# Performance work log

Measured on AMD Instinct MI355X. Metric: run time of the kernel, lower is better.

Reference implementation:

```python
import jax, jax.numpy as jnp
import numpy as np

D_MODEL = 512
PROJ = 2 * D_MODEL  # 1024
N_STATES = 32
KSIZE = 4
LN_EPS = 1e-3  # keras LayerNormalization default epsilon


def setup_inputs() -> dict:
    key = jax.random.key(0)
    ks = jax.random.split(key, 16)
    B, L = 2, 2048
    s_in = 1.0 / np.sqrt(D_MODEL)
    s_pr = 1.0 / np.sqrt(PROJ)
    x = jax.random.normal(ks[0], (B, L, D_MODEL), dtype=jnp.float32)
    # LayerNorm params
    ln_gamma = jnp.ones((D_MODEL,), jnp.float32)
    ln_beta = jnp.zeros((D_MODEL,), jnp.float32)
    # dense1 / dense2: d_model -> proj
    W1 = jax.random.normal(ks[1], (D_MODEL, PROJ), jnp.float32) * s_in
    b1 = jnp.zeros((PROJ,), jnp.float32)
    W2 = jax.random.normal(ks[2], (D_MODEL, PROJ), jnp.float32) * s_in
    b2 = jnp.zeros((PROJ,), jnp.float32)
    # depthwise causal conv1d: kernel (K, 1, PROJ) in WIO layout, groups=PROJ
    conv_k = jax.random.normal(ks[3], (KSIZE, 1, PROJ), jnp.float32) * 0.5
    conv_b = jnp.zeros((PROJ,), jnp.float32)
    # SSM params
    A_log = jnp.log(jnp.broadcast_to(jnp.arange(1, N_STATES + 1, dtype=jnp.float32), (PROJ, N_STATES)))
    D_skip = jnp.ones((PROJ,), jnp.float32)
    WB = jax.random.normal(ks[4], (PROJ, N_STATES), jnp.float32) * s_pr
    bB = jnp.zeros((N_STATES,), jnp.float32)
    WC = jax.random.normal(ks[5], (PROJ, N_STATES), jnp.float32) * s_pr
    bC = jnp.zeros((N_STATES,), jnp.float32)
    Wd = jax.random.normal(ks[6], (PROJ, PROJ), jnp.float32) * s_pr
    bd = jnp.zeros((PROJ,), jnp.float32)
    # dense3: proj -> d_model
    W3 = jax.random.normal(ks[7], (PROJ, D_MODEL), jnp.float32) * s_pr
    b3 = jnp.zeros((D_MODEL,), jnp.float32)
    return dict(x=x, ln_gamma=ln_gamma, ln_beta=ln_beta, W1=W1, b1=b1, W2=W2, b2=b2,
                conv_k=conv_k, conv_b=conv_b, A_log=A_log, D_skip=D_skip,
                WB=WB, bB=bB, WC=WC, bC=bC, Wd=Wd, bd=bd, W3=W3, b3=b3)


def _layernorm(x, gamma, beta):
    mu = jnp.mean(x, axis=-1, keepdims=True)
    var = jnp.mean(jnp.square(x - mu), axis=-1, keepdims=True)
    return (x - mu) * jax.lax.rsqrt(var + LN_EPS) * gamma + beta


def _causal_dwconv(x, k, b):
    # x: [B,L,C], k: [K,1,C], depthwise causal conv (left-pad K-1)
    y = jax.lax.conv_general_dilated(
        x, k, window_strides=(1,), padding=[(KSIZE - 1, 0)],
        dimension_numbers=('NWC', 'WIO', 'NWC'), feature_group_count=PROJ)
    return y + b


def _selective_scan(u, delta, A, Bm, Cm, D_skip):
    # u, delta: [B,L,D]; A: [D,N]; Bm, Cm: [B,L,N]; D_skip: [D]
    deltaA = jnp.einsum('bld,dn->bldn', delta, A)                 # [B,L,D,N]
    deltaBu = jnp.einsum('bld,bld,bln->bldn', delta, u, Bm)        # [B,L,D,N]
    # shift deltaA left by one along L, zero at the end (pad trick in source)
    shifted = jnp.concatenate([deltaA[:, 1:], jnp.zeros_like(deltaA[:, :1])], axis=1)
    # reversed cumsum along L, then exp
    e = jnp.exp(jnp.flip(jnp.cumsum(jnp.flip(shifted, axis=1), axis=1), axis=1))
    xs = jnp.cumsum(deltaBu * e, axis=1) / (e + 1e-12)
    y = jnp.einsum('bldn,bln->bld', xs, Cm)
    return y + u * D_skip


def reference(x, ln_gamma, ln_beta, W1, b1, W2, b2, conv_k, conv_b,
              A_log, D_skip, WB, bB, WC, bC, Wd, bd, W3, b3):
    h = _layernorm(x, ln_gamma, ln_beta)
    x1 = h @ W1 + b1                      # [B,L,PROJ]
    x1 = _causal_dwconv(x1, conv_k, conv_b)
    x1 = jax.nn.silu(x1)
    A = -jnp.exp(A_log)                    # [PROJ,N]
    Cm = x1 @ WC + bC                      # [B,L,N]
    Bm = x1 @ WB + bB                      # [B,L,N]
    delta = jax.nn.softplus(x1 @ Wd + bd)  # [B,L,PROJ]
    y = _selective_scan(x1, delta, A, Bm, Cm, D_skip)
    x2 = jax.nn.silu(h @ W2 + b2)
    out = (y * x2) @ W3 + b3 + x           # residual; dropout is identity at inference
    return out
```

## Files before the change

kernel.cpp:

```cpp
#include <hip/hip_runtime.h>
#include <stdint.h>

#define L_SEQ 2048
#define BATCH 2
#define DMODEL 512
#define PROJ 1024
#define NST 32
#define NCATU 1088
#define ROWS (BATCH*L_SEQ)
#define THRESH 50.0f

typedef float f32x4 __attribute__((ext_vector_type(4)));
typedef short short8 __attribute__((ext_vector_type(8)));

__device__ inline float bf2f(unsigned short u){ uint32_t x=((uint32_t)u)<<16; float f; __builtin_memcpy(&f,&x,4); return f; }
__device__ inline unsigned short f2bf(float f){ uint32_t x; __builtin_memcpy(&x,&f,4); uint32_t r=x+0x7FFFu+((x>>16)&1u); return (unsigned short)(r>>16); }
__device__ inline float siluf(float x){ return x/(1.f+__expf(-x)); }
__device__ inline float softplusf(float x){ return x>20.f? x : log1pf(__expf(x)); }

#define AS1(p) ((const __attribute__((address_space(1))) void*)(p))
#define AS3(p) ((__attribute__((address_space(3))) void*)(p))

template<int N> __device__ inline void wait_vmcnt(){
  if constexpr (N==0)      asm volatile("s_waitcnt vmcnt(0)" ::: "memory");
  else if constexpr (N==4) asm volatile("s_waitcnt vmcnt(4)" ::: "memory");
  else if constexpr (N==8) asm volatile("s_waitcnt vmcnt(8)" ::: "memory");
  else                     asm volatile("s_waitcnt vmcnt(12)" ::: "memory");
}

__global__ __launch_bounds__(256)
void prep_ln_kernel(const float* __restrict__ W1, const float* __restrict__ b1,
                    const float* __restrict__ W2, const float* __restrict__ b2,
                    const float* __restrict__ Wd, const float* __restrict__ bd,
                    const float* __restrict__ WB, const float* __restrict__ bB,
                    const float* __restrict__ WC, const float* __restrict__ bC,
                    const float* __restrict__ W3,
                    unsigned short* __restrict__ W12t, unsigned short* __restrict__ Wcatt,
                    unsigned short* __restrict__ W3t, float* __restrict__ bias12,
                    float* __restrict__ biascat,
                    const float* __restrict__ x, const float* __restrict__ ln_g,
                    const float* __restrict__ ln_b, unsigned short* __restrict__ H)
{
  __shared__ float tile[32][33];
  int bid = blockIdx.x;
  int lx = threadIdx.x & 31, ly = threadIdx.x >> 5;
  if (bid < 1024) {
    int kt = bid & 15, nt = bid >> 4;
    int k0 = kt*32, n0 = nt*32;
    const float* S = (n0 < 1024) ? W1 : W2;
    int nc = (n0 < 1024) ? n0 : n0 - 1024;
#pragma unroll
    for (int i=0;i<4;i++)
      tile[ly+i*8][lx] = S[(size_t)(k0+ly+i*8)*1024 + nc + lx];
    __syncthreads();
#pragma unroll
    for (int i=0;i<4;i++)
      W12t[(size_t)(n0+ly+i*8)*512 + k0 + lx] = f2bf(tile[lx][ly+i*8]);
    return;
  }
  if (bid < 2112) {
    int t = bid - 1024;
    int kt = t & 31, nt = t >> 5;
    int k0 = kt*32, n0 = nt*32;
#pragma unroll
    for (int i=0;i<4;i++){
      int k = k0 + ly + i*8;
      float v;
      if (n0 < 1024)       v = Wd[(size_t)k*1024 + n0 + lx];
      else if (n0 == 1024) v = WB[(size_t)k*32 + lx];
      else                 v = WC[(size_t)k*32 + lx];
      tile[ly+i*8][lx] = v;
    }
    __syncthreads();
#pragma unroll
    for (int i=0;i<4;i++)
      Wcatt[(size_t)(n0+ly+i*8)*1024 + k0 + lx] = f2bf(tile[lx][ly+i*8]);
    return;
  }
  if (bid < 2624) {
    int t = bid - 2112;
    int kt = t & 31, nt = t >> 5;
    int k0 = kt*32, n0 = nt*32;
#pragma unroll
    for (int i=0;i<4;i++)
      tile[ly+i*8][lx] = W3[(size_t)(k0+ly+i*8)*512 + n0 + lx];
    __syncthreads();
#pragma unroll
    for (int i=0;i<4;i++)
      W3t[(size_t)(n0+ly+i*8)*1024 + k0 + lx] = f2bf(tile[lx][ly+i*8]);
    return;
  }
  if (bid < 2637) {
    int j = (bid - 2624)*256 + threadIdx.x;
    if (j < 2048) { bias12[j] = (j < 1024) ? b1[j] : b2[j-1024]; return; }
    j -= 2048;
    if (j < NCATU) biascat[j] = (j < 1024) ? bd[j] : (j < 1056) ? bB[j-1024] : bC[j-1056];
    return;
  }
  int row = (bid - 2637)*4 + (threadIdx.x >> 6);
  int lane = threadIdx.x & 63;
  const float4* xr = (const float4*)(x + (size_t)row*DMODEL);
  float4 v0 = xr[lane];
  float4 v1 = xr[lane+64];
  float s = v0.x+v0.y+v0.z+v0.w + v1.x+v1.y+v1.z+v1.w;
  float q = v0.x*v0.x+v0.y*v0.y+v0.z*v0.z+v0.w*v0.w
          + v1.x*v1.x+v1.y*v1.y+v1.z*v1.z+v1.w*v1.w;
#pragma unroll
  for (int m=32;m>0;m>>=1){ s += __shfl_xor(s,m); q += __shfl_xor(q,m); }
  float mu = s*(1.f/DMODEL);
  float var = q*(1.f/DMODEL) - mu*mu;
  float rs = rsqrtf(var + 1e-3f);
  int c0 = lane*4, c1 = 256 + lane*4;
  float4 g0 = *(const float4*)&ln_g[c0]; float4 g1 = *(const float4*)&ln_g[c1];
  float4 t0 = *(const float4*)&ln_b[c0]; float4 t1 = *(const float4*)&ln_b[c1];
  ushort4 o0, o1;
  o0.x = f2bf((v0.x-mu)*rs*g0.x + t0.x);
  o0.y = f2bf((v0.y-mu)*rs*g0.y + t0.y);
  o0.z = f2bf((v0.z-mu)*rs*g0.z + t0.z);
  o0.w = f2bf((v0.w-mu)*rs*g0.w + t0.w);
  o1.x = f2bf((v1.x-mu)*rs*g1.x + t1.x);
  o1.y = f2bf((v1.y-mu)*rs*g1.y + t1.y);
  o1.z = f2bf((v1.z-mu)*rs*g1.z + t1.z);
  o1.w = f2bf((v1.w-mu)*rs*g1.w + t1.w);
  *(ushort4*)&H[(size_t)row*DMODEL + c0] = o0;
  *(ushort4*)&H[(size_t)row*DMODEL + c1] = o1;
}

template<int MODE>
__global__ __launch_bounds__(256)
void gemm64(const unsigned short* __restrict__ A, const unsigned short* __restrict__ Bt,
            void* __restrict__ Cv, void* __restrict__ Cv2, const float* __restrict__ bias,
            int M, int N, int K, int Kfull)
{
  constexpr int BK = 64;
  constexpr int LPT = 4;
  __shared__ unsigned short As[3][64*BK];
  __shared__ unsigned short Bs[3][64*BK];
  int tid = threadIdx.x;
  int lane = tid & 63, wid = tid >> 6;
  int wm = wid >> 1, wn = wid & 1;
  int gx = gridDim.x;
  int nwg = gx * gridDim.y;
  int L = blockIdx.y*gx + blockIdx.x;
  int W = (L & 7)*(nwg >> 3) + (L >> 3);
  int bx = W % gx, by = W / gx;
  int m0 = bx*64, n0 = by*64;
  int kofs = blockIdx.z*K;

  f32x4 acc[2][2];
#pragma unroll
  for (int i=0;i<2;i++)
#pragma unroll
    for (int j=0;j<2;j++)
#pragma unroll
      for (int e=0;e<4;e++) acc[i][j][e] = 0.f;

  const unsigned short* ap[2];
  const unsigned short* bp[2];
#pragma unroll
  for (int j=0;j<2;j++){
    int s = tid + j*256;
    int row = s >> 3, kc = ((s & 7) ^ (row & 7)) * 8;
    ap[j] = A + (size_t)(m0+row)*Kfull + kofs + kc;
    bp[j] = Bt + (size_t)(n0+row)*Kfull + kofs + kc;
  }
  auto stage = [&](int buf){
#pragma unroll
    for (int j=0;j<2;j++){
      __builtin_amdgcn_global_load_lds(AS1(ap[j]), AS3(&As[buf][(size_t)(j*256 + wid*64)*8]), 16, 0, 0);
      ap[j] += BK;
    }
#pragma unroll
    for (int j=0;j<2;j++){
      __builtin_amdgcn_global_load_lds(AS1(bp[j]), AS3(&Bs[buf][(size_t)(j*256 + wid*64)*8]), 16, 0, 0);
      bp[j] += BK;
    }
  };
  stage(0); stage(1);
  int T = K/BK;
  int rb = 0, wb = 2;
  int r = lane & 15, kb = lane >> 4;
  for (int t = 0; t < T; ++t) {
    if (t+1 < T) wait_vmcnt<LPT>();
    else         wait_vmcnt<0>();
    __builtin_amdgcn_s_barrier();
    if (t+2 < T) { stage(wb); wb = (wb==2)?0:wb+1; }
#pragma unroll
    for (int ks=0; ks<2; ++ks) {
      int cx = (ks*4 + kb) ^ (r & 7);
      short8 af[2], bfr[2];
#pragma unroll
      for (int i=0;i<2;i++) af[i]  = *(const short8*)&As[rb][((wm*32 + i*16 + r)*8 + cx)*8];
#pragma unroll
      for (int j=0;j<2;j++) bfr[j] = *(const short8*)&Bs[rb][((wn*32 + j*16 + r)*8 + cx)*8];
      __builtin_amdgcn_s_setprio(1);
#pragma unroll
      for (int i=0;i<2;i++)
#pragma unroll
        for (int j=0;j<2;j++)
          acc[i][j] = __builtin_amdgcn_mfma_f32_16x16x32_bf16(af[i], bfr[j], acc[i][j], 0,0,0);
      __builtin_amdgcn_s_setprio(0);
    }
    rb = (rb==2)?0:rb+1;
  }
  int rr = (lane >> 4)*4, cc = lane & 15;
#pragma unroll
  for (int i=0;i<2;i++)
#pragma unroll
    for (int j=0;j<2;j++) {
      int col = n0 + wn*32 + j*16 + cc;
#pragma unroll
      for (int e=0;e<4;e++) {
        int row = m0 + wm*32 + i*16 + rr + e;
        float v = acc[i][j][e];
        if constexpr (MODE == 1) {
          v += bias[col];
          if (col < 1024) ((unsigned short*)Cv)[(size_t)row*1024 + col] = f2bf(v);
          else            ((unsigned short*)Cv2)[(size_t)row*1024 + col - 1024] = f2bf(siluf(v));
        } else if constexpr (MODE == 2) {
          v += bias[row];
          if (row < 1024) v = softplusf(v);
          ((float*)Cv)[(size_t)row*N + col] = v;
        } else {
          ((float*)Cv)[(size_t)blockIdx.z*M*N + (size_t)row*N + col] = v;
        }
      }
    }
}

__global__ __launch_bounds__(256)
void reduce_kernel(const float* __restrict__ P, const float* __restrict__ x,
                   const float* __restrict__ b3, float* __restrict__ out)
{
  size_t i = ((size_t)blockIdx.x*256 + threadIdx.x)*4;
  int col = (int)(i & 511);
  float4 a = *(const float4*)&P[i];
  float4 b = *(const float4*)&P[(size_t)ROWS*512 + i];
  float4 xv = *(const float4*)&x[i];
  float4 bv = *(const float4*)&b3[col];
  float4 o;
  o.x = a.x + b.x + xv.x + bv.x;
  o.y = a.y + b.y + xv.y + bv.y;
  o.z = a.z + b.z + xv.z + bv.z;
  o.w = a.w + b.w + xv.w + bv.w;
  *(float4*)&out[i] = o;
}

__global__ __launch_bounds__(256)
void conv_silu_kernel(const unsigned short* __restrict__ P12n, const float* __restrict__ ck,
                      const float* __restrict__ cb, unsigned short* __restrict__ ubf)
{
  int gid = blockIdx.x*256 + threadIdx.x;
  int c = (gid & 255)*4;
  int row = gid >> 8;
  int l = row & (L_SEQ-1);
  float4 bv = *(const float4*)&cb[c];
  float r0=bv.x, r1=bv.y, r2=bv.z, r3=bv.w;
#pragma unroll
  for (int t=0;t<4;t++){
    int lsrc = l - 3 + t;
    if (lsrc >= 0) {
      ushort4 xv = *(const ushort4*)&P12n[(size_t)(row-3+t)*1024 + c];
      float4 kv = *(const float4*)&ck[t*PROJ + c];
      r0 = fmaf(bf2f(xv.x),kv.x,r0);
      r1 = fmaf(bf2f(xv.y),kv.y,r1);
      r2 = fmaf(bf2f(xv.z),kv.z,r2);
      r3 = fmaf(bf2f(xv.w),kv.w,r3);
    }
  }
  ushort4 o;
  o.x=f2bf(siluf(r0)); o.y=f2bf(siluf(r1)); o.z=f2bf(siluf(r2)); o.w=f2bf(siluf(r3));
  *(ushort4*)&ubf[(size_t)row*PROJ + c] = o;
}

__global__ __launch_bounds__(256)
void zmul_pre_kernel(const unsigned short* __restrict__ ubf, const unsigned short* __restrict__ x2bf,
                     const float* __restrict__ Dskip, unsigned short* __restrict__ zbf)
{
  size_t i = ((size_t)blockIdx.x*256 + threadIdx.x)*4;
  int d = (int)(i & (PROJ-1));
  ushort4 uu = *(const ushort4*)&ubf[i];
  ushort4 xx = *(const ushort4*)&x2bf[i];
  float4 Dv = *(const float4*)&Dskip[d];
  ushort4 o;
  o.x = f2bf(bf2f(uu.x)*Dv.x*bf2f(xx.x));
  o.y = f2bf(bf2f(uu.y)*Dv.y*bf2f(xx.y));
  o.z = f2bf(bf2f(uu.z)*Dv.z*bf2f(xx.z));
  o.w = f2bf(bf2f(uu.w)*Dv.w*bf2f(xx.w));
  *(ushort4*)&zbf[i] = o;
}

__global__ __launch_bounds__(256)
void sscan_kernel(const float* __restrict__ CT, const unsigned short* __restrict__ ubf,
                  const unsigned short* __restrict__ x2bf, const float* __restrict__ Dskip,
                  const float* __restrict__ A_log, unsigned short* __restrict__ zbf)
{
  __shared__ float suf8sh[8][256];
  int tid = threadIdx.x;
  int n = tid & 31, gsub = tid >> 5;
  int G = blockIdx.x*8 + gsub;
  int b = G >> 10, d = G & 1023;
  const float* dT = CT + (size_t)d*ROWS + b*L_SEQ;

  float mysum = 0.f;
  {
    const float4* c4 = (const float4*)(dT + n*64);
    for (int it=0; it<16; ++it){ float4 v = c4[it]; mysum += v.x+v.y+v.z+v.w; }
  }
  float incl = mysum;
#pragma unroll
  for (int dlt=1; dlt<32; dlt<<=1){ float t = __shfl_up(incl, dlt, 32); if (n >= dlt) incl += t; }
  float Tot = __shfl(incl, 31, 32);
  float excl = incl - mysum;
  int cnt = 0;
  {
    const float4* c4 = (const float4*)(dT + n*64);
    float run = excl;
    for (int it=0; it<16; ++it){
      float4 v = c4[it];
      if ((it & 1) == 0) suf8sh[gsub][n*8 + (it>>1)] = Tot - run;
      cnt += (Tot - run >= THRESH); run += v.x;
      cnt += (Tot - run >= THRESH); run += v.y;
      cnt += (Tot - run >= THRESH); run += v.z;
      cnt += (Tot - run >= THRESH); run += v.w;
    }
  }
#pragma unroll
  for (int m=16;m>0;m>>=1) cnt += __shfl_xor(cnt, m, 32);
  int myl0 = cnt > 0 ? cnt-1 : 0;
  __syncthreads();

  int base = min(myl0, __shfl_xor(myl0, 32)) & ~7;
  float np1 = __expf(A_log[d*NST + n]);
  float Ds = Dskip[d];
  const float* Br = CT + (size_t)(1024+n)*ROWS + b*L_SEQ;
  const float* Cr = CT + (size_t)(1056+n)*ROWS + b*L_SEQ;
  const unsigned short* ub = ubf + (size_t)b*L_SEQ*PROJ + d;
  const unsigned short* xb = x2bf + (size_t)b*L_SEQ*PROJ + d;
  unsigned short* zb = zbf + (size_t)b*L_SEQ*PROJ + d;
  float s = 0.f;
  for (int l = base; l < L_SEQ; l += 8) {
    float4 d0 = *(const float4*)&dT[l];
    float4 d1 = *(const float4*)&dT[l+4];
    float4 B0 = *(const float4*)&Br[l];
    float4 B1 = *(const float4*)&Br[l+4];
    float4 C0 = *(const float4*)&Cr[l];
    float4 C1 = *(const float4*)&Cr[l+4];
    float uu[8], xx[8];
#pragma unroll
    for (int t=0;t<8;t++) uu[t] = bf2f(ub[(size_t)(l+t)*PROJ]);
#pragma unroll
    for (int t=0;t<8;t++) xx[t] = bf2f(xb[(size_t)(l+t)*PROJ]);
    float sufv = suf8sh[gsub][l >> 3];
    float dl[8] = {d0.x,d0.y,d0.z,d0.w,d1.x,d1.y,d1.z,d1.w};
    float Bv[8] = {B0.x,B0.y,B0.z,B0.w,B1.x,B1.y,B1.z,B1.w};
    float Cv[8] = {C0.x,C0.y,C0.z,C0.w,C1.x,C1.y,C1.z,C1.w};
    float cum = 0.f;
#pragma unroll
    for (int t=0;t<8;t++){
      cum += dl[t];
      float decay = __expf(-dl[t]*np1);
      s = fmaf(decay, s, dl[t]*uu[t]*Bv[t]);
      float gte = 1.f/(1.f + 1e-12f*__expf(np1*(sufv - cum)));
      float contrib = s*gte*Cv[t];
#pragma unroll
      for (int m=16;m>0;m>>=1) contrib += __shfl_xor(contrib, m);
      if (n == 0)
        zb[(size_t)(l+t)*PROJ] = f2bf((contrib + uu[t]*Ds)*xx[t]);
    }
  }
}

extern "C" void kernel_launch(void* const* d_in, const int* in_sizes, int n_in,
                              void* d_out, int out_size, void* d_ws, size_t ws_size,
                              hipStream_t stream)
{
  const float* x     = (const float*)d_in[0];
  const float* ln_g  = (const float*)d_in[1];
  const float* ln_b  = (const float*)d_in[2];
  const float* W1    = (const float*)d_in[3];
  const float* b1    = (const float*)d_in[4];
  const float* W2    = (const float*)d_in[5];
  const float* b2    = (const float*)d_in[6];
  const float* convk = (const float*)d_in[7];
  const float* convb = (const float*)d_in[8];
  const float* A_log = (const float*)d_in[9];
  const float* Dskip = (const float*)d_in[10];
  const float* WB    = (const float*)d_in[11];
  const float* bB    = (const float*)d_in[12];
  const float* WC    = (const float*)d_in[13];
  const float* bC    = (const float*)d_in[14];
  const float* Wd    = (const float*)d_in[15];
  const float* bd    = (const float*)d_in[16];
  const float* W3    = (const float*)d_in[17];
  const float* b3    = (const float*)d_in[18];

  char* w = (char*)d_ws;
  auto alloc = [&](size_t bytes){ char* p = w; w += (bytes + 255) & ~(size_t)255; return p; };
  unsigned short* Hbf    = (unsigned short*)alloc((size_t)ROWS*DMODEL*2);
  unsigned short* W12t   = (unsigned short*)alloc((size_t)2048*512*2);
  unsigned short* Wcatt  = (unsigned short*)alloc((size_t)NCATU*1024*2);
  unsigned short* W3t    = (unsigned short*)alloc((size_t)512*1024*2);
  float*          bias12 = (float*)alloc(2048*4);
  float*          biascat= (float*)alloc(NCATU*4);
  unsigned short* P12n   = (unsigned short*)alloc((size_t)ROWS*1024*2);
  unsigned short* ubf    = (unsigned short*)alloc((size_t)ROWS*PROJ*2);
  unsigned short* x2bf   = (unsigned short*)alloc((size_t)ROWS*PROJ*2);
  float*          CT     = (float*)alloc((size_t)NCATU*ROWS*4);
  unsigned short* zbf    = (unsigned short*)alloc((size_t)ROWS*PROJ*2);
  float*          Pp     = (float*)alloc((size_t)2*ROWS*512*4);

  prep_ln_kernel<<<3661, 256, 0, stream>>>(W1,b1,W2,b2,Wd,bd,WB,bB,WC,bC,W3,
                                           W12t,Wcatt,W3t,bias12,biascat,
                                           x, ln_g, ln_b, Hbf);

  dim3 g1(ROWS/64, 2048/64);
  gemm64<1><<<g1, 256, 0, stream>>>(Hbf, W12t, P12n, x2bf, bias12, ROWS, 2048, DMODEL, DMODEL);

  conv_silu_kernel<<<ROWS*256/256, 256, 0, stream>>>(P12n, convk, convb, ubf);

  zmul_pre_kernel<<<(ROWS*PROJ/4)/256, 256, 0, stream>>>(ubf, x2bf, Dskip, zbf);

  dim3 g2(NCATU/64, ROWS/64);
  gemm64<2><<<g2, 256, 0, stream>>>(Wcatt, ubf, CT, nullptr, biascat, NCATU, ROWS, PROJ, PROJ);

  sscan_kernel<<<2048/8, 256, 0, stream>>>(CT, ubf, x2bf, Dskip, A_log, zbf);

  dim3 g3(ROWS/64, 512/64, 2);
  gemm64<5><<<g3, 256, 0, stream>>>(zbf, W3t, Pp, nullptr, b3, ROWS, 512, 512, PROJ);
  reduce_kernel<<<(ROWS*512/4)/256, 256, 0, stream>>>(Pp, x, b3, (float*)d_out);
}
```

Baseline: 154.9 us.

## Parallelize selective scan over sequence chunks and fuse skip-only prefill into scan

```diff
diff --git a/kernel.cpp b/kernel.cpp
--- a/kernel.cpp
+++ b/kernel.cpp
@@ -274,63 +274,52 @@
 }
 
 __global__ __launch_bounds__(256)
-void zmul_pre_kernel(const unsigned short* __restrict__ ubf, const unsigned short* __restrict__ x2bf,
-                     const float* __restrict__ Dskip, unsigned short* __restrict__ zbf)
-{
-  size_t i = ((size_t)blockIdx.x*256 + threadIdx.x)*4;
-  int d = (int)(i & (PROJ-1));
-  ushort4 uu = *(const ushort4*)&ubf[i];
-  ushort4 xx = *(const ushort4*)&x2bf[i];
-  float4 Dv = *(const float4*)&Dskip[d];
-  ushort4 o;
-  o.x = f2bf(bf2f(uu.x)*Dv.x*bf2f(xx.x));
-  o.y = f2bf(bf2f(uu.y)*Dv.y*bf2f(xx.y));
-  o.z = f2bf(bf2f(uu.z)*Dv.z*bf2f(xx.z));
-  o.w = f2bf(bf2f(uu.w)*Dv.w*bf2f(xx.w));
-  *(ushort4*)&zbf[i] = o;
-}
-
-__global__ __launch_bounds__(256)
 void sscan_kernel(const float* __restrict__ CT, const unsigned short* __restrict__ ubf,
                   const unsigned short* __restrict__ x2bf, const float* __restrict__ Dskip,
                   const float* __restrict__ A_log, unsigned short* __restrict__ zbf)
 {
-  __shared__ float suf8sh[8][256];
+  __shared__ float ps[256];
+  __shared__ float suf8sh[256];
+  __shared__ int   cs[256];
+  __shared__ float Alds[8][32];
+  __shared__ float Slds[8][32];
+  __shared__ int baseSh;
   int tid = threadIdx.x;
-  int n = tid & 31, gsub = tid >> 5;
-  int G = blockIdx.x*8 + gsub;
+  int G = blockIdx.x;
   int b = G >> 10, d = G & 1023;
   const float* dT = CT + (size_t)d*ROWS + b*L_SEQ;
 
-  float mysum = 0.f;
-  {
-    const float4* c4 = (const float4*)(dT + n*64);
-    for (int it=0; it<16; ++it){ float4 v = c4[it]; mysum += v.x+v.y+v.z+v.w; }
-  }
-  float incl = mysum;
-#pragma unroll
-  for (int dlt=1; dlt<32; dlt<<=1){ float t = __shfl_up(incl, dlt, 32); if (n >= dlt) incl += t; }
-  float Tot = __shfl(incl, 31, 32);
-  float excl = incl - mysum;
-  int cnt = 0;
-  {
-    const float4* c4 = (const float4*)(dT + n*64);
-    float run = excl;
-    for (int it=0; it<16; ++it){
-      float4 v = c4[it];
-      if ((it & 1) == 0) suf8sh[gsub][n*8 + (it>>1)] = Tot - run;
-      cnt += (Tot - run >= THRESH); run += v.x;
-      cnt += (Tot - run >= THRESH); run += v.y;
-      cnt += (Tot - run >= THRESH); run += v.z;
-      cnt += (Tot - run >= THRESH); run += v.w;
-    }
-  }
-#pragma unroll
-  for (int m=16;m>0;m>>=1) cnt += __shfl_xor(cnt, m, 32);
-  int myl0 = cnt > 0 ? cnt-1 : 0;
+  float4 a0 = *(const float4*)&dT[tid*8];
+  float4 a1 = *(const float4*)&dT[tid*8+4];
+  float vals[8] = {a0.x,a0.y,a0.z,a0.w,a1.x,a1.y,a1.z,a1.w};
+  float part = 0.f;
+#pragma unroll
+  for (int i=0;i<8;i++) part += vals[i];
+  ps[tid] = part; __syncthreads();
+  for (int off=1; off<256; off<<=1){
+    float v = (tid >= off) ? ps[tid-off] : 0.f;
+    __syncthreads();
+    ps[tid] += v;
+    __syncthreads();
+  }
+  float Tot = ps[255];
+  float prefx = ps[tid] - part;
+  suf8sh[tid] = Tot - prefx;
+  int cnt = 0; float run = prefx;
+#pragma unroll
+  for (int i=0;i<8;i++){ cnt += (Tot - run >= THRESH) ? 1 : 0; run += vals[i]; }
+  cs[tid] = cnt; __syncthreads();
+  for (int off=128; off>0; off>>=1){ if (tid < off) cs[tid] += cs[tid+off]; __syncthreads(); }
+  if (tid == 0) {
+    int total = cs[0];
+    int l0 = total > 0 ? total-1 : 0;
+    baseSh = l0 & ~7;
+  }
   __syncthreads();
-
-  int base = min(myl0, __shfl_xor(myl0, 32)) & ~7;
+  int base = baseSh;
+
+  int n = tid & 31, seg = tid >> 5;
+  int segStart = seg*256, segEnd = segStart + 256;
   float np1 = __expf(A_log[d*NST + n]);
   float Ds = Dskip[d];
   const float* Br = CT + (size_t)(1024+n)*ROWS + b*L_SEQ;
@@ -338,35 +327,85 @@
   const unsigned short* ub = ubf + (size_t)b*L_SEQ*PROJ + d;
   const unsigned short* xb = x2bf + (size_t)b*L_SEQ*PROJ + d;
   unsigned short* zb = zbf + (size_t)b*L_SEQ*PROJ + d;
-  float s = 0.f;
-  for (int l = base; l < L_SEQ; l += 8) {
-    float4 d0 = *(const float4*)&dT[l];
-    float4 d1 = *(const float4*)&dT[l+4];
-    float4 B0 = *(const float4*)&Br[l];
-    float4 B1 = *(const float4*)&Br[l+4];
-    float4 C0 = *(const float4*)&Cr[l];
-    float4 C1 = *(const float4*)&Cr[l+4];
-    float uu[8], xx[8];
-#pragma unroll
-    for (int t=0;t<8;t++) uu[t] = bf2f(ub[(size_t)(l+t)*PROJ]);
-#pragma unroll
-    for (int t=0;t<8;t++) xx[t] = bf2f(xb[(size_t)(l+t)*PROJ]);
-    float sufv = suf8sh[gsub][l >> 3];
-    float dl[8] = {d0.x,d0.y,d0.z,d0.w,d1.x,d1.y,d1.z,d1.w};
-    float Bv[8] = {B0.x,B0.y,B0.z,B0.w,B1.x,B1.y,B1.z,B1.w};
-    float Cv[8] = {C0.x,C0.y,C0.z,C0.w,C1.x,C1.y,C1.z,C1.w};
-    float cum = 0.f;
-#pragma unroll
-    for (int t=0;t<8;t++){
-      cum += dl[t];
-      float decay = __expf(-dl[t]*np1);
-      s = fmaf(decay, s, dl[t]*uu[t]*Bv[t]);
-      float gte = 1.f/(1.f + 1e-12f*__expf(np1*(sufv - cum)));
-      float contrib = s*gte*Cv[t];
-#pragma unroll
-      for (int m=16;m>0;m>>=1) contrib += __shfl_xor(contrib, m);
-      if (n == 0)
-        zb[(size_t)(l+t)*PROJ] = f2bf((contrib + uu[t]*Ds)*xx[t]);
+
+  {
+    int fillEnd = min(segEnd, base);
+    int r0 = segStart + n*8;
+    if (r0 < fillEnd) {
+#pragma unroll
+      for (int i=0;i<8;i++){
+        int r = r0 + i;
+        float u = bf2f(ub[(size_t)r*PROJ]);
+        float x2 = bf2f(xb[(size_t)r*PROJ]);
+        zb[(size_t)r*PROJ] = f2bf(u*Ds*x2);
+      }
+    }
+  }
+
+  bool active = segEnd > base;
+  int sFirst = base >> 8;
+  int lstart = max(segStart, base);
+
+  if (active && seg < 7) {
+    float s = 0.f, Ap = 1.f;
+    for (int l = lstart; l < segEnd; l += 8) {
+      float4 d0 = *(const float4*)&dT[l];
+      float4 d1 = *(const float4*)&dT[l+4];
+      float4 B0 = *(const float4*)&Br[l];
+      float4 B1 = *(const float4*)&Br[l+4];
+      float uu[8];
+#pragma unroll
+      for (int t=0;t<8;t++) uu[t] = bf2f(ub[(size_t)(l+t)*PROJ]);
+      float dl[8] = {d0.x,d0.y,d0.z,d0.w,d1.x,d1.y,d1.z,d1.w};
+      float Bv[8] = {B0.x,B0.y,B0.z,B0.w,B1.x,B1.y,B1.z,B1.w};
+#pragma unroll
+      for (int t=0;t<8;t++){
+        float decay = __expf(-dl[t]*np1);
+        s = fmaf(decay, s, dl[t]*uu[t]*Bv[t]);
+        Ap *= decay;
+      }
+    }
+    Alds[seg][n] = Ap; Slds[seg][n] = s;
+  }
+  __syncthreads();
+
+  float sin = 0.f;
+  if (active) {
+    for (int c = sFirst; c < seg; ++c)
+      sin = fmaf(Alds[c][n], sin, Slds[c][n]);
+  }
+
+  if (active) {
+    float s = sin;
+    for (int l = lstart; l < segEnd; l += 8) {
+      float4 d0 = *(const float4*)&dT[l];
+      float4 d1 = *(const float4*)&dT[l+4];
+      float4 B0 = *(const float4*)&Br[l];
+      float4 B1 = *(const float4*)&Br[l+4];
+      float4 C0 = *(const float4*)&Cr[l];
+      float4 C1 = *(const float4*)&Cr[l+4];
+      float uu[8], xx[8];
+#pragma unroll
+      for (int t=0;t<8;t++) uu[t] = bf2f(ub[(size_t)(l+t)*PROJ]);
+#pragma unroll
+      for (int t=0;t<8;t++) xx[t] = bf2f(xb[(size_t)(l+t)*PROJ]);
+      float sufv = suf8sh[l >> 3];
+      float dl[8] = {d0.x,d0.y,d0.z,d0.w,d1.x,d1.y,d1.z,d1.w};
+      float Bv[8] = {B0.x,B0.y,B0.z,B0.w,B1.x,B1.y,B1.z,B1.w};
+      float Cv[8] = {C0.x,C0.y,C0.z,C0.w,C1.x,C1.y,C1.z,C1.w};
+      float cum = 0.f;
+#pragma unroll
+      for (int t=0;t<8;t++){
+        cum += dl[t];
+        float decay = __expf(-dl[t]*np1);
+        s = fmaf(decay, s, dl[t]*uu[t]*Bv[t]);
+        float gte = 1.f/(1.f + 1e-12f*__expf(np1*(sufv - cum)));
+        float contrib = s*gte*Cv[t];
+#pragma unroll
+        for (int m=16;m>0;m>>=1) contrib += __shfl_xor(contrib, m);
+        if (n == 0)
+          zb[(size_t)(l+t)*PROJ] = f2bf((contrib + uu[t]*Ds)*xx[t]);
+      }
     }
   }
 }
@@ -419,12 +458,10 @@
 
   conv_silu_kernel<<<ROWS*256/256, 256, 0, stream>>>(P12n, convk, convb, ubf);
 
-  zmul_pre_kernel<<<(ROWS*PROJ/4)/256, 256, 0, stream>>>(ubf, x2bf, Dskip, zbf);
-
   dim3 g2(NCATU/64, ROWS/64);
   gemm64<2><<<g2, 256, 0, stream>>>(Wcatt, ubf, CT, nullptr, biascat, NCATU, ROWS, PROJ, PROJ);
 
-  sscan_kernel<<<2048/8, 256, 0, stream>>>(CT, ubf, x2bf, Dskip, A_log, zbf);
+  sscan_kernel<<<2048, 256, 0, stream>>>(CT, ubf, x2bf, Dskip, A_log, zbf);
 
   dim3 g3(ROWS/64, 512/64, 2);
   gemm64<5><<<g3, 256, 0, stream>>>(zbf, W3t, Pp, nullptr, b3, ROWS, 512, 512, PROJ);
```

Measured after the change: 196.1 us. 26.6% more time.

## Transpose u and x2 for contiguous scan loads and use full wavefront per channel

Applied to the files above, without the earlier changes.

```diff
diff --git a/kernel.cpp b/kernel.cpp
--- a/kernel.cpp
+++ b/kernel.cpp
@@ -274,6 +274,24 @@
 }
 
 __global__ __launch_bounds__(256)
+void utrans_kernel(const unsigned short* __restrict__ u, const unsigned short* __restrict__ x2,
+                   unsigned short* __restrict__ uT, unsigned short* __restrict__ x2T)
+{
+  __shared__ unsigned short tile[32][33];
+  const unsigned short* src = blockIdx.z ? x2 : u;
+  unsigned short* dst = blockIdx.z ? x2T : uT;
+  int r0 = blockIdx.x*32, c0 = blockIdx.y*32;
+  int lx = threadIdx.x & 31, ly = threadIdx.x >> 5;
+#pragma unroll
+  for (int i=0;i<4;i++)
+    tile[ly+i*8][lx] = src[(size_t)(r0+ly+i*8)*1024 + c0 + lx];
+  __syncthreads();
+#pragma unroll
+  for (int i=0;i<4;i++)
+    dst[(size_t)(c0+ly+i*8)*ROWS + r0 + lx] = tile[lx][ly+i*8];
+}
+
+__global__ __launch_bounds__(256)
 void zmul_pre_kernel(const unsigned short* __restrict__ ubf, const unsigned short* __restrict__ x2bf,
                      const float* __restrict__ Dskip, unsigned short* __restrict__ zbf)
 {
@@ -291,70 +309,72 @@
 }
 
 __global__ __launch_bounds__(256)
-void sscan_kernel(const float* __restrict__ CT, const unsigned short* __restrict__ ubf,
-                  const unsigned short* __restrict__ x2bf, const float* __restrict__ Dskip,
+void sscan_kernel(const float* __restrict__ CT, const unsigned short* __restrict__ uT,
+                  const unsigned short* __restrict__ x2T, const float* __restrict__ Dskip,
                   const float* __restrict__ A_log, unsigned short* __restrict__ zbf)
 {
-  __shared__ float suf8sh[8][256];
   int tid = threadIdx.x;
-  int n = tid & 31, gsub = tid >> 5;
-  int G = blockIdx.x*8 + gsub;
+  int lane = tid & 63;
+  int G = blockIdx.x*4 + (tid >> 6);
   int b = G >> 10, d = G & 1023;
   const float* dT = CT + (size_t)d*ROWS + b*L_SEQ;
 
-  float mysum = 0.f;
-  {
-    const float4* c4 = (const float4*)(dT + n*64);
-    for (int it=0; it<16; ++it){ float4 v = c4[it]; mysum += v.x+v.y+v.z+v.w; }
-  }
-  float incl = mysum;
-#pragma unroll
-  for (int dlt=1; dlt<32; dlt<<=1){ float t = __shfl_up(incl, dlt, 32); if (n >= dlt) incl += t; }
-  float Tot = __shfl(incl, 31, 32);
-  float excl = incl - mysum;
+  float4 v4[8];
+#pragma unroll
+  for (int it=0; it<8; ++it) v4[it] = *(const float4*)&dT[lane*32 + it*4];
+  float p1 = v4[0].x+v4[0].y+v4[0].z+v4[0].w + v4[1].x+v4[1].y+v4[1].z+v4[1].w;
+  float p2 = p1 + v4[2].x+v4[2].y+v4[2].z+v4[2].w + v4[3].x+v4[3].y+v4[3].z+v4[3].w;
+  float p3 = p2 + v4[4].x+v4[4].y+v4[4].z+v4[4].w + v4[5].x+v4[5].y+v4[5].z+v4[5].w;
+  float lsum = p3 + v4[6].x+v4[6].y+v4[6].z+v4[6].w + v4[7].x+v4[7].y+v4[7].z+v4[7].w;
+  float incl = lsum;
+#pragma unroll
+  for (int dlt=1; dlt<64; dlt<<=1){ float t = __shfl_up(incl, dlt, 64); if (lane >= dlt) incl += t; }
+  float Tot = __shfl(incl, 63, 64);
+  float excl = incl - lsum;
+  float bnd0 = Tot - excl;
+  float bnd1 = Tot - (excl + p1);
+  float bnd2 = Tot - (excl + p2);
+  float bnd3 = Tot - (excl + p3);
   int cnt = 0;
   {
-    const float4* c4 = (const float4*)(dT + n*64);
     float run = excl;
-    for (int it=0; it<16; ++it){
-      float4 v = c4[it];
-      if ((it & 1) == 0) suf8sh[gsub][n*8 + (it>>1)] = Tot - run;
-      cnt += (Tot - run >= THRESH); run += v.x;
-      cnt += (Tot - run >= THRESH); run += v.y;
-      cnt += (Tot - run >= THRESH); run += v.z;
-      cnt += (Tot - run >= THRESH); run += v.w;
-    }
-  }
-#pragma unroll
-  for (int m=16;m>0;m>>=1) cnt += __shfl_xor(cnt, m, 32);
-  int myl0 = cnt > 0 ? cnt-1 : 0;
-  __syncthreads();
-
-  int base = min(myl0, __shfl_xor(myl0, 32)) & ~7;
+    const float* vf = (const float*)v4;
+#pragma unroll
+    for (int i=0;i<32;i++){ cnt += (Tot - run >= THRESH) ? 1 : 0; run += vf[i]; }
+  }
+#pragma unroll
+  for (int m=32;m>0;m>>=1) cnt += __shfl_xor(cnt, m, 64);
+  int l0 = cnt > 0 ? cnt-1 : 0;
+  int base = l0 & ~7;
+
+  int n = lane & 31;
   float np1 = __expf(A_log[d*NST + n]);
   float Ds = Dskip[d];
   const float* Br = CT + (size_t)(1024+n)*ROWS + b*L_SEQ;
   const float* Cr = CT + (size_t)(1056+n)*ROWS + b*L_SEQ;
-  const unsigned short* ub = ubf + (size_t)b*L_SEQ*PROJ + d;
-  const unsigned short* xb = x2bf + (size_t)b*L_SEQ*PROJ + d;
+  const unsigned short* ub = uT  + (size_t)d*ROWS + b*L_SEQ;
+  const unsigned short* xb = x2T + (size_t)d*ROWS + b*L_SEQ;
   unsigned short* zb = zbf + (size_t)b*L_SEQ*PROJ + d;
   float s = 0.f;
   for (int l = base; l < L_SEQ; l += 8) {
+    int j = l >> 3, owner = j >> 2, q = j & 3;
+    float bsel = (q==0) ? bnd0 : (q==1) ? bnd1 : (q==2) ? bnd2 : bnd3;
+    float sufv = __shfl(bsel, owner, 64);
     float4 d0 = *(const float4*)&dT[l];
     float4 d1 = *(const float4*)&dT[l+4];
     float4 B0 = *(const float4*)&Br[l];
     float4 B1 = *(const float4*)&Br[l+4];
     float4 C0 = *(const float4*)&Cr[l];
     float4 C1 = *(const float4*)&Cr[l+4];
-    float uu[8], xx[8];
-#pragma unroll
-    for (int t=0;t<8;t++) uu[t] = bf2f(ub[(size_t)(l+t)*PROJ]);
-#pragma unroll
-    for (int t=0;t<8;t++) xx[t] = bf2f(xb[(size_t)(l+t)*PROJ]);
-    float sufv = suf8sh[gsub][l >> 3];
+    ushort4 u0 = *(const ushort4*)&ub[l], u1 = *(const ushort4*)&ub[l+4];
+    ushort4 x0 = *(const ushort4*)&xb[l], x1 = *(const ushort4*)&xb[l+4];
     float dl[8] = {d0.x,d0.y,d0.z,d0.w,d1.x,d1.y,d1.z,d1.w};
     float Bv[8] = {B0.x,B0.y,B0.z,B0.w,B1.x,B1.y,B1.z,B1.w};
     float Cv[8] = {C0.x,C0.y,C0.z,C0.w,C1.x,C1.y,C1.z,C1.w};
+    float uu[8] = {bf2f(u0.x),bf2f(u0.y),bf2f(u0.z),bf2f(u0.w),
+                   bf2f(u1.x),bf2f(u1.y),bf2f(u1.z),bf2f(u1.w)};
+    float xx[8] = {bf2f(x0.x),bf2f(x0.y),bf2f(x0.z),bf2f(x0.w),
+                   bf2f(x1.x),bf2f(x1.y),bf2f(x1.z),bf2f(x1.w)};
     float cum = 0.f;
 #pragma unroll
     for (int t=0;t<8;t++){
@@ -365,7 +385,7 @@
       float contrib = s*gte*Cv[t];
 #pragma unroll
       for (int m=16;m>0;m>>=1) contrib += __shfl_xor(contrib, m);
-      if (n == 0)
+      if (lane == 0)
         zb[(size_t)(l+t)*PROJ] = f2bf((contrib + uu[t]*Ds)*xx[t]);
     }
   }
@@ -406,6 +426,8 @@
   unsigned short* P12n   = (unsigned short*)alloc((size_t)ROWS*1024*2);
   unsigned short* ubf    = (unsigned short*)alloc((size_t)ROWS*PROJ*2);
   unsigned short* x2bf   = (unsigned short*)alloc((size_t)ROWS*PROJ*2);
+  unsigned short* uT     = (unsigned short*)alloc((size_t)PROJ*ROWS*2);
+  unsigned short* x2T    = (unsigned short*)alloc((size_t)PROJ*ROWS*2);
   float*          CT     = (float*)alloc((size_t)NCATU*ROWS*4);
   unsigned short* zbf    = (unsigned short*)alloc((size_t)ROWS*PROJ*2);
   float*          Pp     = (float*)alloc((size_t)2*ROWS*512*4);
@@ -419,12 +441,15 @@
 
   conv_silu_kernel<<<ROWS*256/256, 256, 0, stream>>>(P12n, convk, convb, ubf);
 
+  dim3 gt(ROWS/32, PROJ/32, 2);
+  utrans_kernel<<<gt, 256, 0, stream>>>(ubf, x2bf, uT, x2T);
+
   zmul_pre_kernel<<<(ROWS*PROJ/4)/256, 256, 0, stream>>>(ubf, x2bf, Dskip, zbf);
 
   dim3 g2(NCATU/64, ROWS/64);
   gemm64<2><<<g2, 256, 0, stream>>>(Wcatt, ubf, CT, nullptr, biascat, NCATU, ROWS, PROJ, PROJ);
 
-  sscan_kernel<<<2048/8, 256, 0, stream>>>(CT, ubf, x2bf, Dskip, A_log, zbf);
+  sscan_kernel<<<512, 256, 0, stream>>>(CT, uT, x2T, Dskip, A_log, zbf);
 
   dim3 g3(ROWS/64, 512/64, 2);
   gemm64<5><<<g3, 256, 0, stream>>>(zbf, W3t, Pp, nullptr, b3, ROWS, 512, 512, PROJ);
```

Measured after the change: 158.6 us. +2.4%, slower.
